# Performance work log

Measured on AMD Instinct MI355X. Metric: run time of the kernel, lower is better.

The kernel has to match this reference:

```python
import jax, jax.numpy as jnp
import numpy as np

B, S, D_IN, D_OUT = 4, 4096, 768, 64


def setup_inputs() -> dict:
    key = jax.random.key(0)
    kx, kq, kk, kv = jax.random.split(key, 4)
    x = jax.random.normal(kx, (B, S, D_IN), dtype=jnp.float32)
    # kaiming-uniform-ish scale for weights
    bound = 1.0 / np.sqrt(D_IN)
    Wq = jax.random.uniform(kq, (D_IN, D_OUT), jnp.float32, -bound, bound)
    Wk = jax.random.uniform(kk, (D_IN, D_OUT), jnp.float32, -bound, bound)
    Wv = jax.random.uniform(kv, (D_IN, D_OUT), jnp.float32, -bound, bound)
    return {"x": x, "Wq": Wq, "Wk": Wk, "Wv": Wv}


def reference(x, Wq, Wk, Wv):
    # QKV projections (qkv_bias=False)
    q = jnp.einsum("bsi,io->bso", x, Wq)  # [B,S,D_OUT]
    k = jnp.einsum("bsi,io->bso", x, Wk)
    v = jnp.einsum("bsi,io->bso", x, Wv)
    # scores [B,S,S], causal mask (upper triangle excl. diag -> -inf)
    scores = jnp.einsum("bqd,bkd->bqk", q, k)
    num_tokens = x.shape[1]
    causal = jnp.triu(jnp.ones((num_tokens, num_tokens), dtype=bool), k=1)
    scores = jnp.where(causal[None, :, :], -jnp.inf, scores)
    scale = 1.0 / np.sqrt(k.shape[-1]).astype(np.float32)
    attn = jax.nn.softmax(scores * scale, axis=-1)
    # dropout: eval mode -> identity (module's custom Dropout is a no-op when not training)
    ctx = jnp.einsum("bqk,bkv->bqv", attn, v)  # [B,S,D_OUT]
    return ctx
```

## Files before the change

### kernel.cpp

```cpp
#include <hip/hip_runtime.h>
#include <stdint.h>

#define KSTEPS 24
#define TOKENS 16384

typedef short short8 __attribute__((ext_vector_type(8)));
typedef float fx4 __attribute__((ext_vector_type(4)));
typedef unsigned short u16;
typedef u16 u16x4 __attribute__((ext_vector_type(4)));

static __device__ __forceinline__ u16 f2bf(float f) {
  union { float f; unsigned u; } v; v.f = f;
  return (u16)((v.u + 0x7fffu + ((v.u >> 16) & 1u)) >> 16);
}

static __device__ __forceinline__ fx4 mfma16(short8 a, short8 b, fx4 c) {
  return __builtin_amdgcn_mfma_f32_16x16x32_bf16(a, b, c, 0, 0, 0);
}

static __device__ __forceinline__ void async16(const void* g, void* l) {
  __builtin_amdgcn_global_load_lds(
      (const __attribute__((address_space(1))) void*)g,
      (__attribute__((address_space(3))) void*)(unsigned int)(uintptr_t)l,
      16, 0, 0);
}

__global__ void prep_w_kernel(const float* __restrict__ Wq, const float* __restrict__ Wk,
                              const float* __restrict__ Wv, u16* __restrict__ wfrag) {
  int idx  = blockIdx.x * 256 + threadIdx.x;
  int lane = idx & 63;
  int fid  = idx >> 6;
  int nt   = fid & 3;
  int ks   = (fid >> 2) % KSTEPS;
  int mat  = fid / (KSTEPS * 4);
  const float* W = (mat == 0) ? Wq : (mat == 1) ? Wk : Wv;
  int n  = nt * 16 + (lane & 15);
  int k0 = ks * 32 + (lane >> 4) * 8;
  short8 out;
#pragma unroll
  for (int j = 0; j < 8; j++) out[j] = (short)f2bf(W[(size_t)(k0 + j) * 64 + n]);
  *(short8*)(wfrag + (size_t)idx * 8) = out;
}

__global__ __launch_bounds__(256) void proj_kernel(const float* __restrict__ x,
                                                   const u16* __restrict__ wfrag,
                                                   u16* __restrict__ qb,
                                                   u16* __restrict__ kb,
                                                   u16* __restrict__ vT) {
  __shared__ float xs[2][32 * 32];
  __shared__ u16  Ws[2][12 * 512];

  int w = threadIdx.x >> 6, lane = threadIdx.x & 63;
  int ln = lane & 15, quad = lane >> 4;
  int rw = w >> 1, cs = w & 1;
  int s0 = blockIdx.x * 32;

  fx4 acc[6];
#pragma unroll
  for (int j = 0; j < 6; j++) acc[j] = (fx4){0.f, 0.f, 0.f, 0.f};

  int srow  = w * 8 + (lane >> 3);
  int slot  = lane & 7;
  int chunk = slot ^ (srow & 7);
  const float* xsrc = x + (size_t)(s0 + srow) * 768 + chunk * 4;

#pragma unroll
  for (int m = 0; m < 3; m++)
    async16(wfrag + ((size_t)(m * KSTEPS + 0) * 256 + w * 64 + lane) * 8,
            (char*)Ws[0] + m * 4096 + w * 1024 + lane * 16);
  async16(xsrc, (char*)xs[0] + w * 1024 + lane * 16);

  int r = rw * 16 + ln;
  for (int ks = 0; ks < KSTEPS; ks++) {
    __syncthreads();
    if (ks < KSTEPS - 1) {
      int buf = (ks + 1) & 1;
#pragma unroll
      for (int m = 0; m < 3; m++)
        async16(wfrag + ((size_t)(m * KSTEPS + ks + 1) * 256 + w * 64 + lane) * 8,
                (char*)Ws[buf] + m * 4096 + w * 1024 + lane * 16);
      async16(xsrc + (ks + 1) * 32, (char*)xs[buf] + w * 1024 + lane * 16);
    }
    const float* xb = xs[ks & 1];
    const u16*  wb = Ws[ks & 1];
    int sl0 = (2 * quad)     ^ (r & 7);
    int sl1 = (2 * quad + 1) ^ (r & 7);
    fx4 xa = *(const fx4*)(xb + r * 32 + sl0 * 4);
    fx4 xv = *(const fx4*)(xb + r * 32 + sl1 * 4);
    short8 af;
#pragma unroll
    for (int j = 0; j < 4; j++) { af[j] = (short)f2bf(xa[j]); af[4 + j] = (short)f2bf(xv[j]); }
#pragma unroll
    for (int j = 0; j < 6; j++) {
      short8 bf = *(const short8*)(wb + (cs * 6 + j) * 512 + lane * 8);
      acc[j] = mfma16(af, bf, acc[j]);
    }
  }

  int tok0 = s0 + rw * 16 + quad * 4;
#pragma unroll
  for (int j = 0; j < 6; j++) {
    int f = cs * 6 + j;
    int d = (f & 3) * 16 + ln;
    if (f < 4) {
#pragma unroll
      for (int reg = 0; reg < 4; reg++)
        qb[(size_t)(tok0 + reg) * 64 + d] = f2bf(acc[j][reg] * 0.180336887f);
    } else if (f < 8) {
#pragma unroll
      for (int reg = 0; reg < 4; reg++)
        kb[(size_t)(tok0 + reg) * 64 + d] = f2bf(acc[j][reg]);
    } else {
      int b = tok0 >> 12, s = tok0 & 4095;
      u16x4 vp;
#pragma unroll
      for (int reg = 0; reg < 4; reg++) vp[reg] = f2bf(acc[j][reg]);
      *(u16x4*)(vT + ((size_t)b * 64 + d) * 4096 + s) = vp;
    }
  }
}

__global__ __launch_bounds__(256) void attn_kernel(const u16* __restrict__ qb,
                                                   const u16* __restrict__ kb,
                                                   const u16* __restrict__ vT,
                                                   float* __restrict__ o0g,
                                                   float* __restrict__ po12,
                                                   float* __restrict__ mlb) {
  __shared__ u16 Kstg[2][4096];
  __shared__ u16 Vstg[2][4096];
  __shared__ u16 Ps[4][16 * 72];

  int w = threadIdx.x >> 6, lane = threadIdx.x & 63;
  int ln = lane & 15, quad = lane >> 4;
  int band = 63 - blockIdx.x;
  int b = blockIdx.y, z = blockIdx.z;
  int q0 = band * 64;

  const u16* qbb = qb + (size_t)b * 4096 * 64;
  const u16* kbb = kb + (size_t)b * 4096 * 64;
  const u16* vtb = vT + (size_t)b * 64 * 4096;

  short8 qf0 = *(const short8*)(qbb + (size_t)(q0 + w * 16 + ln) * 64 + quad * 8);
  short8 qf1 = *(const short8*)(qbb + (size_t)(q0 + w * 16 + ln) * 64 + 32 + quad * 8);

  short8 ones;
#pragma unroll
  for (int j = 0; j < 8; j++) ones[j] = (short)0x3F80;

  fx4 o[4];
#pragma unroll
  for (int nt2 = 0; nt2 < 4; nt2++) o[nt2] = (fx4){0.f, 0.f, 0.f, 0.f};
  float l_i[4] = {0.f, 0.f, 0.f, 0.f};

  int n = band + 1;
  int c = (n + 2) / 3;
  int lo = z * c; if (lo > n) lo = n;
  int hi = lo + c; if (hi > n) hi = n;

  if (lo < hi) {
#pragma unroll
    for (int j = 0; j < 2; j++) {
      int cc = (w * 2 + j) * 64 + lane;
      int row = cc >> 3, slot = cc & 7, sw = (slot ^ (row & 7)) * 8;
      async16(kbb + ((size_t)lo * 64 + row) * 64 + sw, (char*)Kstg[0] + (w * 2 + j) * 1024);
      async16(vtb + (size_t)row * 4096 + lo * 64 + sw, (char*)Vstg[0] + (w * 2 + j) * 1024);
    }
  }

  for (int t = lo; t < hi; t++) {
    __syncthreads();
    if (t + 1 < hi) {
      int nb = (t - lo + 1) & 1;
#pragma unroll
      for (int j = 0; j < 2; j++) {
        int cc = (w * 2 + j) * 64 + lane;
        int row = cc >> 3, slot = cc & 7, sw = (slot ^ (row & 7)) * 8;
        async16(kbb + ((size_t)(t + 1) * 64 + row) * 64 + sw,
                (char*)Kstg[nb] + (w * 2 + j) * 1024);
        async16(vtb + (size_t)row * 4096 + (t + 1) * 64 + sw,
                (char*)Vstg[nb] + (w * 2 + j) * 1024);
      }
    }
    const u16* Kb = Kstg[(t - lo) & 1];
    const u16* Vb = Vstg[(t - lo) & 1];

    fx4 sA[4];
#pragma unroll
    for (int nt = 0; nt < 4; nt++) {
      int row = nt * 16 + ln;
      int s0_ = quad ^ (row & 7), s1_ = (quad + 4) ^ (row & 7);
      short8 kf0 = *(const short8*)(Kb + (row * 8 + s0_) * 8);
      short8 kf1 = *(const short8*)(Kb + (row * 8 + s1_) * 8);
      sA[nt] = mfma16(qf0, kf0, (fx4){0.f, 0.f, 0.f, 0.f});
      sA[nt] = mfma16(qf1, kf1, sA[nt]);
    }

    if (t == n - 1) {
#pragma unroll
      for (int nt = 0; nt < 4; nt++)
#pragma unroll
        for (int reg = 0; reg < 4; reg++) {
          int col = t * 64 + nt * 16 + ln;
          int rowg = q0 + w * 16 + quad * 4 + reg;
          if (col > rowg) sA[nt][reg] = -1e30f;
        }
    }

#pragma unroll
    for (int nt = 0; nt < 4; nt++)
#pragma unroll
      for (int reg = 0; reg < 4; reg++)
        Ps[w][(quad * 4 + reg) * 72 + nt * 16 + ln] =
            f2bf(__builtin_amdgcn_exp2f(sA[nt][reg]));

    short8 pf0 = *(const short8*)(&Ps[w][ln * 72 + quad * 8]);
    short8 pf1 = *(const short8*)(&Ps[w][ln * 72 + 32 + quad * 8]);

    fx4 lacc = mfma16(pf0, ones, (fx4){0.f, 0.f, 0.f, 0.f});
    lacc = mfma16(pf1, ones, lacc);
#pragma unroll
    for (int reg = 0; reg < 4; reg++) l_i[reg] += lacc[reg];

#pragma unroll
    for (int nt2 = 0; nt2 < 4; nt2++) {
      int row = nt2 * 16 + ln;
      int s0_ = quad ^ (row & 7), s1_ = (quad + 4) ^ (row & 7);
      short8 vf0 = *(const short8*)(Vb + (row * 8 + s0_) * 8);
      short8 vf1 = *(const short8*)(Vb + (row * 8 + s1_) * 8);
      o[nt2] = mfma16(pf0, vf0, o[nt2]);
      o[nt2] = mfma16(pf1, vf1, o[nt2]);
    }
  }

  float* dst = (z == 0) ? o0g : (po12 + (size_t)(z - 1) * 4 * 4096 * 64);
#pragma unroll
  for (int nt2 = 0; nt2 < 4; nt2++)
#pragma unroll
    for (int reg = 0; reg < 4; reg++) {
      int rowg = q0 + w * 16 + quad * 4 + reg;
      dst[((size_t)b * 4096 + rowg) * 64 + nt2 * 16 + ln] = o[nt2][reg];
    }
  if (ln == 0) {
#pragma unroll
    for (int reg = 0; reg < 4; reg++) {
      int rowg = q0 + w * 16 + quad * 4 + reg;
      mlb[((size_t)z * 4 + b) * 4096 + rowg] = l_i[reg];
    }
  }
}

__global__ __launch_bounds__(256) void merge_kernel(float* __restrict__ out,
                                                    const float* __restrict__ po12,
                                                    const float* __restrict__ mlb) {
  int qt = blockIdx.x, b = blockIdx.y;
  int r = threadIdx.x >> 3;
  int c = (threadIdx.x & 7) * 8;
  size_t row = (size_t)b * 4096 + qt * 32 + r;
  float l = mlb[row];
#pragma unroll
  for (int z = 1; z < 3; z++) l += mlb[(size_t)z * 4 * 4096 + row];
  float inv = 1.0f / l;
  float* op = out + row * 64 + c;
  fx4 u0 = *(fx4*)op, u1 = *(fx4*)(op + 4);
#pragma unroll
  for (int z = 1; z < 3; z++) {
    const float* pp = po12 + (size_t)(z - 1) * 4 * 4096 * 64 + row * 64 + c;
    fx4 v0 = *(const fx4*)pp, v1 = *(const fx4*)(pp + 4);
#pragma unroll
    for (int j = 0; j < 4; j++) { u0[j] += v0[j]; u1[j] += v1[j]; }
  }
#pragma unroll
  for (int j = 0; j < 4; j++) { u0[j] *= inv; u1[j] *= inv; }
  *(fx4*)op = u0;
  *(fx4*)(op + 4) = u1;
}

extern "C" void kernel_launch(void* const* d_in, const int* in_sizes, int n_in,
                              void* d_out, int out_size, void* d_ws, size_t ws_size,
                              hipStream_t stream) {
  const float* x  = (const float*)d_in[0];
  const float* Wq = (const float*)d_in[1];
  const float* Wk = (const float*)d_in[2];
  const float* Wv = (const float*)d_in[3];

  u16* qbw = (u16*)d_ws;
  u16* kbw = qbw + (size_t)TOKENS * 64;
  u16* vtw = kbw + (size_t)TOKENS * 64;
  u16* wfr = vtw + (size_t)TOKENS * 64;
  float* po12 = (float*)(wfr + (size_t)3 * KSTEPS * 256 * 8);
  float* mlb = po12 + (size_t)2 * 4 * 4096 * 64;

  prep_w_kernel<<<72, 256, 0, stream>>>(Wq, Wk, Wv, wfr);
  proj_kernel<<<TOKENS / 32, 256, 0, stream>>>(x, wfr, qbw, kbw, vtw);
  attn_kernel<<<dim3(64, 4, 3), 256, 0, stream>>>(qbw, kbw, vtw,
                                                  (float*)d_out, po12, mlb);
  merge_kernel<<<dim3(128, 4), 256, 0, stream>>>((float*)d_out, po12, mlb);
}
```

Baseline: 142.3 us.

## Use 128-row query bands with 8 waves and 6-way KV split

The attention kernel now processes 128 query rows per block with 8 waves (512 threads), so each staged K/V tile is shared by twice as many query rows. The KV range is split six ways instead of three, and waves skip tiles that lie entirely above their causal diagonal. The merge kernel now sums five partial buffers instead of two, which means more workspace traffic. The P-to-bf16 conversion also switches to a cheaper round-half-up, which changes rounding slightly.

```diff
diff --git a/kernel.cpp b/kernel.cpp
--- a/kernel.cpp
+++ b/kernel.cpp
@@ -12,6 +12,11 @@
 static __device__ __forceinline__ u16 f2bf(float f) {
   union { float f; unsigned u; } v; v.f = f;
   return (u16)((v.u + 0x7fffu + ((v.u >> 16) & 1u)) >> 16);
+}
+
+static __device__ __forceinline__ u16 p2bf(float f) {
+  union { float f; unsigned u; } v; v.f = f;
+  return (u16)((v.u + 0x8000u) >> 16);
 }
 
 static __device__ __forceinline__ fx4 mfma16(short8 a, short8 b, fx4 c) {
@@ -120,28 +125,29 @@
   }
 }
 
-__global__ __launch_bounds__(256) void attn_kernel(const u16* __restrict__ qb,
+__global__ __launch_bounds__(512) void attn_kernel(const u16* __restrict__ qb,
                                                    const u16* __restrict__ kb,
                                                    const u16* __restrict__ vT,
                                                    float* __restrict__ o0g,
-                                                   float* __restrict__ po12,
+                                                   float* __restrict__ po5,
                                                    float* __restrict__ mlb) {
   __shared__ u16 Kstg[2][4096];
   __shared__ u16 Vstg[2][4096];
-  __shared__ u16 Ps[4][16 * 72];
+  __shared__ u16 Ps[8][16 * 72];
 
   int w = threadIdx.x >> 6, lane = threadIdx.x & 63;
   int ln = lane & 15, quad = lane >> 4;
-  int band = 63 - blockIdx.x;
+  int band = 31 - blockIdx.x;
   int b = blockIdx.y, z = blockIdx.z;
-  int q0 = band * 64;
+  int q0 = band * 128;
+  int qw = q0 + w * 16;
 
   const u16* qbb = qb + (size_t)b * 4096 * 64;
   const u16* kbb = kb + (size_t)b * 4096 * 64;
   const u16* vtb = vT + (size_t)b * 64 * 4096;
 
-  short8 qf0 = *(const short8*)(qbb + (size_t)(q0 + w * 16 + ln) * 64 + quad * 8);
-  short8 qf1 = *(const short8*)(qbb + (size_t)(q0 + w * 16 + ln) * 64 + 32 + quad * 8);
+  short8 qf0 = *(const short8*)(qbb + (size_t)(qw + ln) * 64 + quad * 8);
+  short8 qf1 = *(const short8*)(qbb + (size_t)(qw + ln) * 64 + 32 + quad * 8);
 
   short8 ones;
 #pragma unroll
@@ -152,35 +158,27 @@
   for (int nt2 = 0; nt2 < 4; nt2++) o[nt2] = (fx4){0.f, 0.f, 0.f, 0.f};
   float l_i[4] = {0.f, 0.f, 0.f, 0.f};
 
-  int n = band + 1;
-  int c = (n + 2) / 3;
+  int n = 2 * band + 2;
+  int c = (n + 5) / 6;
   int lo = z * c; if (lo > n) lo = n;
   int hi = lo + c; if (hi > n) hi = n;
 
+  int cc = w * 64 + lane;
+  int srow = cc >> 3, sslot = cc & 7, sw_ = (sslot ^ (srow & 7)) * 8;
   if (lo < hi) {
-#pragma unroll
-    for (int j = 0; j < 2; j++) {
-      int cc = (w * 2 + j) * 64 + lane;
-      int row = cc >> 3, slot = cc & 7, sw = (slot ^ (row & 7)) * 8;
-      async16(kbb + ((size_t)lo * 64 + row) * 64 + sw, (char*)Kstg[0] + (w * 2 + j) * 1024);
-      async16(vtb + (size_t)row * 4096 + lo * 64 + sw, (char*)Vstg[0] + (w * 2 + j) * 1024);
-    }
+    async16(kbb + ((size_t)lo * 64 + srow) * 64 + sw_, (char*)Kstg[0] + cc * 16);
+    async16(vtb + (size_t)srow * 4096 + lo * 64 + sw_, (char*)Vstg[0] + cc * 16);
   }
 
   for (int t = lo; t < hi; t++) {
     __syncthreads();
     if (t + 1 < hi) {
       int nb = (t - lo + 1) & 1;
-#pragma unroll
-      for (int j = 0; j < 2; j++) {
-        int cc = (w * 2 + j) * 64 + lane;
-        int row = cc >> 3, slot = cc & 7, sw = (slot ^ (row & 7)) * 8;
-        async16(kbb + ((size_t)(t + 1) * 64 + row) * 64 + sw,
-                (char*)Kstg[nb] + (w * 2 + j) * 1024);
-        async16(vtb + (size_t)row * 4096 + (t + 1) * 64 + sw,
-                (char*)Vstg[nb] + (w * 2 + j) * 1024);
-      }
-    }
+      async16(kbb + ((size_t)(t + 1) * 64 + srow) * 64 + sw_, (char*)Kstg[nb] + cc * 16);
+      async16(vtb + (size_t)srow * 4096 + (t + 1) * 64 + sw_, (char*)Vstg[nb] + cc * 16);
+    }
+    if (64 * t > qw + 15) continue;
+
     const u16* Kb = Kstg[(t - lo) & 1];
     const u16* Vb = Vstg[(t - lo) & 1];
 
@@ -195,13 +193,13 @@
       sA[nt] = mfma16(qf1, kf1, sA[nt]);
     }
 
-    if (t == n - 1) {
+    if (64 * t + 63 > qw) {
 #pragma unroll
       for (int nt = 0; nt < 4; nt++)
 #pragma unroll
         for (int reg = 0; reg < 4; reg++) {
           int col = t * 64 + nt * 16 + ln;
-          int rowg = q0 + w * 16 + quad * 4 + reg;
+          int rowg = qw + quad * 4 + reg;
           if (col > rowg) sA[nt][reg] = -1e30f;
         }
     }
@@ -211,7 +209,7 @@
 #pragma unroll
       for (int reg = 0; reg < 4; reg++)
         Ps[w][(quad * 4 + reg) * 72 + nt * 16 + ln] =
-            f2bf(__builtin_amdgcn_exp2f(sA[nt][reg]));
+            p2bf(__builtin_amdgcn_exp2f(sA[nt][reg]));
 
     short8 pf0 = *(const short8*)(&Ps[w][ln * 72 + quad * 8]);
     short8 pf1 = *(const short8*)(&Ps[w][ln * 72 + 32 + quad * 8]);
@@ -232,25 +230,25 @@
     }
   }
 
-  float* dst = (z == 0) ? o0g : (po12 + (size_t)(z - 1) * 4 * 4096 * 64);
+  float* dst = (z == 0) ? o0g : (po5 + (size_t)(z - 1) * 4 * 4096 * 64);
 #pragma unroll
   for (int nt2 = 0; nt2 < 4; nt2++)
 #pragma unroll
     for (int reg = 0; reg < 4; reg++) {
-      int rowg = q0 + w * 16 + quad * 4 + reg;
+      int rowg = qw + quad * 4 + reg;
       dst[((size_t)b * 4096 + rowg) * 64 + nt2 * 16 + ln] = o[nt2][reg];
     }
   if (ln == 0) {
 #pragma unroll
     for (int reg = 0; reg < 4; reg++) {
-      int rowg = q0 + w * 16 + quad * 4 + reg;
+      int rowg = qw + quad * 4 + reg;
       mlb[((size_t)z * 4 + b) * 4096 + rowg] = l_i[reg];
     }
   }
 }
 
 __global__ __launch_bounds__(256) void merge_kernel(float* __restrict__ out,
-                                                    const float* __restrict__ po12,
+                                                    const float* __restrict__ po5,
                                                     const float* __restrict__ mlb) {
   int qt = blockIdx.x, b = blockIdx.y;
   int r = threadIdx.x >> 3;
@@ -258,13 +256,13 @@
   size_t row = (size_t)b * 4096 + qt * 32 + r;
   float l = mlb[row];
 #pragma unroll
-  for (int z = 1; z < 3; z++) l += mlb[(size_t)z * 4 * 4096 + row];
+  for (int z = 1; z < 6; z++) l += mlb[(size_t)z * 4 * 4096 + row];
   float inv = 1.0f / l;
   float* op = out + row * 64 + c;
   fx4 u0 = *(fx4*)op, u1 = *(fx4*)(op + 4);
 #pragma unroll
-  for (int z = 1; z < 3; z++) {
-    const float* pp = po12 + (size_t)(z - 1) * 4 * 4096 * 64 + row * 64 + c;
+  for (int z = 1; z < 6; z++) {
+    const float* pp = po5 + (size_t)(z - 1) * 4 * 4096 * 64 + row * 64 + c;
     fx4 v0 = *(const fx4*)pp, v1 = *(const fx4*)(pp + 4);
 #pragma unroll
     for (int j = 0; j < 4; j++) { u0[j] += v0[j]; u1[j] += v1[j]; }
@@ -287,12 +285,12 @@
   u16* kbw = qbw + (size_t)TOKENS * 64;
   u16* vtw = kbw + (size_t)TOKENS * 64;
   u16* wfr = vtw + (size_t)TOKENS * 64;
-  float* po12 = (float*)(wfr + (size_t)3 * KSTEPS * 256 * 8);
-  float* mlb = po12 + (size_t)2 * 4 * 4096 * 64;
+  float* po5 = (float*)(wfr + (size_t)3 * KSTEPS * 256 * 8);
+  float* mlb = po5 + (size_t)5 * 4 * 4096 * 64;
 
   prep_w_kernel<<<72, 256, 0, stream>>>(Wq, Wk, Wv, wfr);
   proj_kernel<<<TOKENS / 32, 256, 0, stream>>>(x, wfr, qbw, kbw, vtw);
-  attn_kernel<<<dim3(64, 4, 3), 256, 0, stream>>>(qbw, kbw, vtw,
-                                                  (float*)d_out, po12, mlb);
-  merge_kernel<<<dim3(128, 4), 256, 0, stream>>>((float*)d_out, po12, mlb);
-}
+  attn_kernel<<<dim3(32, 4, 6), 512, 0, stream>>>(qbw, kbw, vtw,
+                                                  (float*)d_out, po5, mlb);
+  merge_kernel<<<dim3(128, 4), 256, 0, stream>>>((float*)d_out, po5, mlb);
+}
```

After: 138.6 us. 1.03x faster.
